# Optimization experiments

Measured on AMD Instinct MI355X. Metric: run time of the kernel, lower is better.

## Reference

```python
import jax, jax.numpy as jnp
import numpy as np

N = 1_000_000      # total points
G = 256            # number of interaction clusters (segments)
D_IN = 4           # [energy, x, y, z] per-point features
H1, H2, LATENT = 64, 128, 256
D_OUT = 3          # vertex position dims


def setup_inputs() -> dict:
    key = jax.random.key(0)
    ks = jax.random.split(key, 10)
    point_cloud = jax.random.normal(ks[0], (N, 5), dtype=jnp.float32)
    seg_ids = jnp.sort(jax.random.randint(ks[1], (N,), 0, G, dtype=jnp.int64))
    def lin(k, fan_in, fan_out):
        s = 1.0 / np.sqrt(fan_in)
        return jax.random.uniform(k, (fan_in, fan_out), jnp.float32, -s, s)
    W1 = lin(ks[2], D_IN, H1);   b1 = jnp.zeros((H1,), jnp.float32)
    W2 = lin(ks[3], H1, H2);     b2 = jnp.zeros((H2,), jnp.float32)
    W3 = lin(ks[4], H2, LATENT); b3 = jnp.zeros((LATENT,), jnp.float32)
    Wf = lin(ks[5], LATENT, D_OUT); bf = jnp.zeros((D_OUT,), jnp.float32)
    return {"point_cloud": point_cloud, "W1": W1, "b1": b1, "W2": W2, "b2": b2,
            "W3": W3, "b3": b3, "Wf": Wf, "bf": bf, "seg_ids": seg_ids}


def reference(point_cloud, W1, b1, W2, b2, W3, b3, Wf, bf, seg_ids):
    pos = point_cloud[:, 1:4]          # [N,3]
    x = point_cloud[:, 4:5]            # [N,1] energy
    # --- per-segment centroids (segment mean, single pass) ---
    counts = jax.ops.segment_sum(jnp.ones((pos.shape[0],), pos.dtype), seg_ids,
                                 num_segments=G)                      # [G]
    centroids = jax.ops.segment_sum(pos, seg_ids, num_segments=G)
    centroids = centroids / jnp.maximum(counts, 1.0)[:, None]         # [G,3]
    # --- PointNet encoder: shared per-point MLP + per-segment max-pool ---
    feats = jnp.concatenate([x, pos], axis=1)                         # [N,4]
    h = jax.nn.relu(feats @ W1 + b1)                                  # [N,64]
    h = jax.nn.relu(h @ W2 + b2)                                      # [N,128]
    h = h @ W3 + b3                                                   # [N,256]
    pooled = jax.ops.segment_max(h, seg_ids, num_segments=G)          # [G,256]
    # --- final Linear + Softplus head, added to centroids ---
    out = jax.nn.softplus(pooled @ Wf + bf)                           # [G,3]
    return centroids + out
```

## Files before the change

kernel.cpp:

```cpp
#include <hip/hip_runtime.h>
#include <float.h>

typedef __bf16 bf16x8 __attribute__((ext_vector_type(8)));
typedef __bf16 bf16x4 __attribute__((ext_vector_type(4)));
typedef float  f32x4  __attribute__((ext_vector_type(4)));

#define G      256
#define MT     32
#define H1DIM  64
#define H2DIM  128
#define LAT    256
#define H1PAD  72
#define H2PAD  136

__device__ __forceinline__ unsigned mapf(float f) {
  unsigned u = __float_as_uint(f);
  return (u & 0x80000000u) ? ~u : (u | 0x80000000u);
}
__device__ __forceinline__ float unmapf(unsigned u) {
  return (u & 0x80000000u) ? __uint_as_float(u & 0x7fffffffu) : __uint_as_float(~u);
}

__device__ __forceinline__ void flush4(f32x4 v0, f32x4 v1, f32x4 v2, f32x4 v3,
                                       int s, int w, int q, int nn,
                                       const float* __restrict__ b3,
                                       unsigned* __restrict__ pooled) {
  f32x4 vv[4] = {v0, v1, v2, v3};
  #pragma unroll
  for (int mt = 0; mt < 4; ++mt)
    #pragma unroll
    for (int r = 0; r < 4; ++r) {
      int feat = w * 64 + mt * 16 + q * 4 + r;
      float v = vv[mt][r] + b3[feat];
      v = fmaxf(v, __shfl_xor(v, 1));
      v = fmaxf(v, __shfl_xor(v, 2));
      v = fmaxf(v, __shfl_xor(v, 4));
      v = fmaxf(v, __shfl_xor(v, 8));
      if (nn == 0) atomicMax(&pooled[s * LAT + feat], mapf(v));
    }
}

__global__ __launch_bounds__(256, 2) void mlp_kernel(
    const float* __restrict__ pc,
    const float* __restrict__ W1, const float* __restrict__ b1,
    const float* __restrict__ W2, const float* __restrict__ b2,
    const float* __restrict__ W3, const float* __restrict__ b3,
    const int* __restrict__ sid,
    unsigned* __restrict__ pooled,
    float* __restrict__ sums,
    int n, int tiles_per_block) {
  __shared__ __align__(16) __bf16 shF[MT][8];
  __shared__ __align__(16) __bf16 sh1[MT][H1PAD];
  __shared__ __align__(16) __bf16 sh2[MT][H2PAD];
  __shared__ int segt[MT];

  const int t  = threadIdx.x;
  const int w  = t >> 6;
  const int lane = t & 63;
  const int q  = lane >> 4;
  const int nn = lane & 15;

  bf16x8 w1f;
  #pragma unroll
  for (int j = 0; j < 8; ++j) {
    int k = q * 8 + j;
    w1f[j] = (k < 4) ? (__bf16)W1[k * H1DIM + w * 16 + nn] : (__bf16)0.f;
  }
  float b1r[4];
  #pragma unroll
  for (int r = 0; r < 4; ++r) b1r[r] = b1[w * 16 + q * 4 + r];

  bf16x8 w2f[2][2];
  float  b2r[2][4];
  #pragma unroll
  for (int mt = 0; mt < 2; ++mt) {
    int m = w * 32 + mt * 16 + nn;
    #pragma unroll
    for (int ks = 0; ks < 2; ++ks)
      #pragma unroll
      for (int j = 0; j < 8; ++j)
        w2f[mt][ks][j] = (__bf16)W2[(ks * 32 + q * 8 + j) * H2DIM + m];
    #pragma unroll
    for (int r = 0; r < 4; ++r) b2r[mt][r] = b2[w * 32 + mt * 16 + q * 4 + r];
  }

  bf16x8 w3f[4][4];
  #pragma unroll
  for (int mt = 0; mt < 4; ++mt) {
    int m = w * 64 + mt * 16 + nn;
    #pragma unroll
    for (int ks = 0; ks < 4; ++ks)
      #pragma unroll
      for (int j = 0; j < 8; ++j)
        w3f[mt][ks][j] = (__bf16)W3[(ks * 32 + q * 8 + j) * LAT + m];
  }

  const f32x4 zero4 = {0.f, 0.f, 0.f, 0.f};
  const bf16x8 zero8 = {};
  const f32x4 neginf4 = {-FLT_MAX, -FLT_MAX, -FLT_MAX, -FLT_MAX};

  f32x4 run[4];
  #pragma unroll
  for (int mt = 0; mt < 4; ++mt) run[mt] = neginf4;

  float cx = 0.f, cy = 0.f, cz = 0.f, cc = 0.f;
  int   cseg = -1;

  const int tile0 = blockIdx.x * tiles_per_block;
  int first = tile0 * MT; if (first > n - 1) first = n - 1;
  int s_cur = sid[first];

  for (int ti = 0; ti < tiles_per_block; ++ti) {
    const int base = (tile0 + ti) * MT;
    if (base >= n) break;

    if (t < MT) {
      int p = base + t;
      bool valid = p < n;
      int pcl = valid ? p : (n - 1);
      const float* pp = pc + (size_t)pcl * 5;
      float fx = pp[4], p1 = pp[1], p2 = pp[2], p3 = pp[3];
      bf16x8 v = {};
      v[0] = (__bf16)fx;
      v[1] = (__bf16)p1;
      v[2] = (__bf16)p2;
      v[3] = (__bf16)p3;
      *reinterpret_cast<bf16x8*>(&shF[t][0]) = v;
      int s = sid[pcl];
      segt[t] = s;
      if (valid) {
        if (s != cseg) {
          if (cc > 0.f) {
            atomicAdd(&sums[cseg * 4 + 0], cx);
            atomicAdd(&sums[cseg * 4 + 1], cy);
            atomicAdd(&sums[cseg * 4 + 2], cz);
            atomicAdd(&sums[cseg * 4 + 3], cc);
          }
          cseg = s; cx = 0.f; cy = 0.f; cz = 0.f; cc = 0.f;
        }
        cx += p1; cy += p2; cz += p3; cc += 1.f;
      }
    }
    __syncthreads();

    {
      f32x4 acc1[2];
      #pragma unroll
      for (int nt = 0; nt < 2; ++nt) {
        bf16x8 ld = *reinterpret_cast<const bf16x8*>(&shF[nt * 16 + nn][0]);
        bf16x8 af = (q == 0) ? ld : zero8;
        acc1[nt] = __builtin_amdgcn_mfma_f32_16x16x32_bf16(w1f, af, zero4, 0, 0, 0);
      }
      #pragma unroll
      for (int nt = 0; nt < 2; ++nt) {
        bf16x4 pk;
        #pragma unroll
        for (int r = 0; r < 4; ++r)
          pk[r] = (__bf16)fmaxf(acc1[nt][r] + b1r[r], 0.f);
        *reinterpret_cast<bf16x4*>(&sh1[nt * 16 + nn][w * 16 + q * 4]) = pk;
      }
    }
    __syncthreads();

    {
      f32x4 acc2[2][2];
      #pragma unroll
      for (int mt = 0; mt < 2; ++mt)
        #pragma unroll
        for (int nt = 0; nt < 2; ++nt) acc2[mt][nt] = zero4;
      #pragma unroll
      for (int ks = 0; ks < 2; ++ks) {
        bf16x8 bfr[2];
        #pragma unroll
        for (int nt = 0; nt < 2; ++nt)
          bfr[nt] = *reinterpret_cast<const bf16x8*>(&sh1[nt * 16 + nn][ks * 32 + q * 8]);
        #pragma unroll
        for (int mt = 0; mt < 2; ++mt)
          #pragma unroll
          for (int nt = 0; nt < 2; ++nt)
            acc2[mt][nt] = __builtin_amdgcn_mfma_f32_16x16x32_bf16(w2f[mt][ks], bfr[nt], acc2[mt][nt], 0, 0, 0);
      }
      #pragma unroll
      for (int mt = 0; mt < 2; ++mt)
        #pragma unroll
        for (int nt = 0; nt < 2; ++nt) {
          bf16x4 pk;
          #pragma unroll
          for (int r = 0; r < 4; ++r)
            pk[r] = (__bf16)fmaxf(acc2[mt][nt][r] + b2r[mt][r], 0.f);
          *reinterpret_cast<bf16x4*>(&sh2[nt * 16 + nn][w * 32 + mt * 16 + q * 4]) = pk;
        }
    }
    __syncthreads();

    f32x4 acc3[4][2];
    #pragma unroll
    for (int mt = 0; mt < 4; ++mt)
      #pragma unroll
      for (int nt = 0; nt < 2; ++nt) acc3[mt][nt] = zero4;
    #pragma unroll
    for (int ks = 0; ks < 4; ++ks) {
      bf16x8 bfr[2];
      #pragma unroll
      for (int nt = 0; nt < 2; ++nt)
        bfr[nt] = *reinterpret_cast<const bf16x8*>(&sh2[nt * 16 + nn][ks * 32 + q * 8]);
      #pragma unroll
      for (int mt = 0; mt < 4; ++mt)
        #pragma unroll
        for (int nt = 0; nt < 2; ++nt)
          acc3[mt][nt] = __builtin_amdgcn_mfma_f32_16x16x32_bf16(w3f[mt][ks], bfr[nt], acc3[mt][nt], 0, 0, 0);
    }

    int smin = segt[0], smax = segt[MT - 1];
    if (smin != s_cur) {
      flush4(run[0], run[1], run[2], run[3], s_cur, w, q, nn, b3, pooled);
      #pragma unroll
      for (int mt = 0; mt < 4; ++mt) run[mt] = neginf4;
      s_cur = smin;
    }
    if (smin == smax) {
      #pragma unroll
      for (int mt = 0; mt < 4; ++mt)
        #pragma unroll
        for (int r = 0; r < 4; ++r)
          run[mt][r] = fmaxf(run[mt][r], fmaxf(acc3[mt][0][r], acc3[mt][1][r]));
    } else {
      int sg0 = segt[nn], sg1 = segt[16 + nn];
      for (int s = smin; s <= smax; ++s) {
        f32x4 tmp[4];
        #pragma unroll
        for (int mt = 0; mt < 4; ++mt)
          #pragma unroll
          for (int r = 0; r < 4; ++r) {
            float v0 = (sg0 == s) ? acc3[mt][0][r] : -FLT_MAX;
            float v1 = (sg1 == s) ? acc3[mt][1][r] : -FLT_MAX;
            tmp[mt][r] = fmaxf(v0, v1);
          }
        if (s < smax) {
          if (s == s_cur) {
            #pragma unroll
            for (int mt = 0; mt < 4; ++mt)
              #pragma unroll
              for (int r = 0; r < 4; ++r) run[mt][r] = fmaxf(run[mt][r], tmp[mt][r]);
            flush4(run[0], run[1], run[2], run[3], s, w, q, nn, b3, pooled);
            #pragma unroll
            for (int mt = 0; mt < 4; ++mt) run[mt] = neginf4;
          } else {
            flush4(tmp[0], tmp[1], tmp[2], tmp[3], s, w, q, nn, b3, pooled);
          }
        } else {
          #pragma unroll
          for (int mt = 0; mt < 4; ++mt)
            #pragma unroll
            for (int r = 0; r < 4; ++r) run[mt][r] = fmaxf(run[mt][r], tmp[mt][r]);
        }
      }
      s_cur = smax;
    }
    __syncthreads();
  }
  flush4(run[0], run[1], run[2], run[3], s_cur, w, q, nn, b3, pooled);

  if (t < MT && cc > 0.f) {
    atomicAdd(&sums[cseg * 4 + 0], cx);
    atomicAdd(&sums[cseg * 4 + 1], cy);
    atomicAdd(&sums[cseg * 4 + 2], cz);
    atomicAdd(&sums[cseg * 4 + 3], cc);
  }
}

__global__ void final_kernel(const float* __restrict__ sums, const unsigned* __restrict__ pooled,
                             const float* __restrict__ Wf, const float* __restrict__ bfv,
                             float* __restrict__ out) {
  __shared__ float red[4][3];
  int g = blockIdx.x;
  int t = threadIdx.x;
  unsigned u = pooled[g * LAT + t];
  float f = u ? unmapf(u) : 0.f;
  float s0 = f * Wf[t * 3 + 0];
  float s1 = f * Wf[t * 3 + 1];
  float s2 = f * Wf[t * 3 + 2];
  #pragma unroll
  for (int off = 1; off < 64; off <<= 1) {
    s0 += __shfl_xor(s0, off);
    s1 += __shfl_xor(s1, off);
    s2 += __shfl_xor(s2, off);
  }
  int wave = t >> 6;
  if ((t & 63) == 0) { red[wave][0] = s0; red[wave][1] = s1; red[wave][2] = s2; }
  __syncthreads();
  if (t < 3) {
    float acc = bfv[t] + red[0][t] + red[1][t] + red[2][t] + red[3][t];
    float sp  = fmaxf(acc, 0.f) + log1pf(expf(-fabsf(acc)));
    float cnt = fmaxf(sums[g * 4 + 3], 1.f);
    float cen = sums[g * 4 + t] / cnt;
    out[g * 3 + t] = cen + sp;
  }
}

extern "C" void kernel_launch(void* const* d_in, const int* in_sizes, int n_in,
                              void* d_out, int out_size, void* d_ws, size_t ws_size,
                              hipStream_t stream) {
  const float* pc  = (const float*)d_in[0];
  const float* W1  = (const float*)d_in[1];
  const float* b1  = (const float*)d_in[2];
  const float* W2  = (const float*)d_in[3];
  const float* b2  = (const float*)d_in[4];
  const float* W3  = (const float*)d_in[5];
  const float* b3  = (const float*)d_in[6];
  const float* Wf  = (const float*)d_in[7];
  const float* bfv = (const float*)d_in[8];
  const int*   sid = (const int*)d_in[9];
  int n = in_sizes[0] / 5;

  float*    sums   = (float*)d_ws;
  unsigned* pooled = (unsigned*)((char*)d_ws + 4096);
  hipMemsetAsync(d_ws, 0, 4096 + (size_t)G * LAT * 4, stream);

  int tiles   = (n + MT - 1) / MT;
  int nblocks = 512;
  int tpb     = (tiles + nblocks - 1) / nblocks;
  mlp_kernel<<<nblocks, 256, 0, stream>>>(pc, W1, b1, W2, b2, W3, b3, sid, pooled, sums, n, tpb);

  final_kernel<<<G, 256, 0, stream>>>(sums, pooled, Wf, bfv, (float*)d_out);
}
```

Measured before the change: 224.9 us.

## Double the point tile to 64 and prefetch next tile's inputs into double-buffered shared memory

Raises the per-iteration tile from 32 to 64 points, so each wave issues more MFMAs per barrier and each weight fragment is reused across more columns. It also double-buffers the input features and segment-id arrays, loading the next tile's point data into registers before the MLP and writing it to the alternate buffer afterwards, removing one barrier per tile and hiding global load latency. The cost is more accumulator registers (acc3 grows to 16 vectors), which may pressure occupancy under launch_bounds(256,2). The host's tiles_per_block or grid size may need to account for the new tile size.

```diff
diff --git a/kernel.cpp b/kernel.cpp
--- a/kernel.cpp
+++ b/kernel.cpp
@@ -6,7 +6,7 @@
 typedef float  f32x4  __attribute__((ext_vector_type(4)));
 
 #define G      256
-#define MT     32
+#define MT     64
 #define H1DIM  64
 #define H2DIM  128
 #define LAT    256
@@ -49,10 +49,10 @@
     unsigned* __restrict__ pooled,
     float* __restrict__ sums,
     int n, int tiles_per_block) {
-  __shared__ __align__(16) __bf16 shF[MT][8];
+  __shared__ __align__(16) __bf16 shF[2][MT][8];
   __shared__ __align__(16) __bf16 sh1[MT][H1PAD];
   __shared__ __align__(16) __bf16 sh2[MT][H2PAD];
-  __shared__ int segt[MT];
+  __shared__ int segt[2][MT];
 
   const int t  = threadIdx.x;
   const int w  = t >> 6;
@@ -110,49 +110,50 @@
   int first = tile0 * MT; if (first > n - 1) first = n - 1;
   int s_cur = sid[first];
 
+  if (t < MT) {
+    int p = tile0 * MT + t;
+    bool valid = p < n;
+    int pcl = valid ? p : (n - 1);
+    const float* pp = pc + (size_t)pcl * 5;
+    float fx = pp[4], p1 = pp[1], p2 = pp[2], p3 = pp[3];
+    bf16x8 v = {};
+    v[0] = (__bf16)fx; v[1] = (__bf16)p1; v[2] = (__bf16)p2; v[3] = (__bf16)p3;
+    *reinterpret_cast<bf16x8*>(&shF[0][t][0]) = v;
+    int s = sid[pcl];
+    segt[0][t] = s;
+    if (valid) { cseg = s; cx = p1; cy = p2; cz = p3; cc = 1.f; }
+  }
+  __syncthreads();
+
+  int cur = 0;
   for (int ti = 0; ti < tiles_per_block; ++ti) {
     const int base = (tile0 + ti) * MT;
     if (base >= n) break;
 
-    if (t < MT) {
-      int p = base + t;
-      bool valid = p < n;
-      int pcl = valid ? p : (n - 1);
+    float pf1 = 0.f, pf2 = 0.f, pf3 = 0.f, pfx = 0.f;
+    int   pfs = 0;
+    bool  pfvalid = false;
+    const int base2 = base + MT;
+    const bool hasNext = (ti + 1 < tiles_per_block) && (base2 < n);
+    if (hasNext && t < MT) {
+      int p = base2 + t;
+      pfvalid = p < n;
+      int pcl = pfvalid ? p : (n - 1);
       const float* pp = pc + (size_t)pcl * 5;
-      float fx = pp[4], p1 = pp[1], p2 = pp[2], p3 = pp[3];
-      bf16x8 v = {};
-      v[0] = (__bf16)fx;
-      v[1] = (__bf16)p1;
-      v[2] = (__bf16)p2;
-      v[3] = (__bf16)p3;
-      *reinterpret_cast<bf16x8*>(&shF[t][0]) = v;
-      int s = sid[pcl];
-      segt[t] = s;
-      if (valid) {
-        if (s != cseg) {
-          if (cc > 0.f) {
-            atomicAdd(&sums[cseg * 4 + 0], cx);
-            atomicAdd(&sums[cseg * 4 + 1], cy);
-            atomicAdd(&sums[cseg * 4 + 2], cz);
-            atomicAdd(&sums[cseg * 4 + 3], cc);
-          }
-          cseg = s; cx = 0.f; cy = 0.f; cz = 0.f; cc = 0.f;
-        }
-        cx += p1; cy += p2; cz += p3; cc += 1.f;
-      }
-    }
-    __syncthreads();
+      pfx = pp[4]; pf1 = pp[1]; pf2 = pp[2]; pf3 = pp[3];
+      pfs = sid[pcl];
+    }
 
     {
-      f32x4 acc1[2];
-      #pragma unroll
-      for (int nt = 0; nt < 2; ++nt) {
-        bf16x8 ld = *reinterpret_cast<const bf16x8*>(&shF[nt * 16 + nn][0]);
+      f32x4 acc1[4];
+      #pragma unroll
+      for (int nt = 0; nt < 4; ++nt) {
+        bf16x8 ld = *reinterpret_cast<const bf16x8*>(&shF[cur][nt * 16 + nn][0]);
         bf16x8 af = (q == 0) ? ld : zero8;
         acc1[nt] = __builtin_amdgcn_mfma_f32_16x16x32_bf16(w1f, af, zero4, 0, 0, 0);
       }
       #pragma unroll
-      for (int nt = 0; nt < 2; ++nt) {
+      for (int nt = 0; nt < 4; ++nt) {
         bf16x4 pk;
         #pragma unroll
         for (int r = 0; r < 4; ++r)
@@ -163,27 +164,27 @@
     __syncthreads();
 
     {
-      f32x4 acc2[2][2];
+      f32x4 acc2[2][4];
       #pragma unroll
       for (int mt = 0; mt < 2; ++mt)
         #pragma unroll
-        for (int nt = 0; nt < 2; ++nt) acc2[mt][nt] = zero4;
+        for (int nt = 0; nt < 4; ++nt) acc2[mt][nt] = zero4;
       #pragma unroll
       for (int ks = 0; ks < 2; ++ks) {
-        bf16x8 bfr[2];
-        #pragma unroll
-        for (int nt = 0; nt < 2; ++nt)
+        bf16x8 bfr[4];
+        #pragma unroll
+        for (int nt = 0; nt < 4; ++nt)
           bfr[nt] = *reinterpret_cast<const bf16x8*>(&sh1[nt * 16 + nn][ks * 32 + q * 8]);
         #pragma unroll
         for (int mt = 0; mt < 2; ++mt)
           #pragma unroll
-          for (int nt = 0; nt < 2; ++nt)
+          for (int nt = 0; nt < 4; ++nt)
             acc2[mt][nt] = __builtin_amdgcn_mfma_f32_16x16x32_bf16(w2f[mt][ks], bfr[nt], acc2[mt][nt], 0, 0, 0);
       }
       #pragma unroll
       for (int mt = 0; mt < 2; ++mt)
         #pragma unroll
-        for (int nt = 0; nt < 2; ++nt) {
+        for (int nt = 0; nt < 4; ++nt) {
           bf16x4 pk;
           #pragma unroll
           for (int r = 0; r < 4; ++r)
@@ -193,25 +194,25 @@
     }
     __syncthreads();
 
-    f32x4 acc3[4][2];
+    f32x4 acc3[4][4];
     #pragma unroll
     for (int mt = 0; mt < 4; ++mt)
       #pragma unroll
-      for (int nt = 0; nt < 2; ++nt) acc3[mt][nt] = zero4;
+      for (int nt = 0; nt < 4; ++nt) acc3[mt][nt] = zero4;
     #pragma unroll
     for (int ks = 0; ks < 4; ++ks) {
-      bf16x8 bfr[2];
-      #pragma unroll
-      for (int nt = 0; nt < 2; ++nt)
+      bf16x8 bfr[4];
+      #pragma unroll
+      for (int nt = 0; nt < 4; ++nt)
         bfr[nt] = *reinterpret_cast<const bf16x8*>(&sh2[nt * 16 + nn][ks * 32 + q * 8]);
       #pragma unroll
       for (int mt = 0; mt < 4; ++mt)
         #pragma unroll
-        for (int nt = 0; nt < 2; ++nt)
+        for (int nt = 0; nt < 4; ++nt)
           acc3[mt][nt] = __builtin_amdgcn_mfma_f32_16x16x32_bf16(w3f[mt][ks], bfr[nt], acc3[mt][nt], 0, 0, 0);
     }
 
-    int smin = segt[0], smax = segt[MT - 1];
+    int smin = segt[cur][0], smax = segt[cur][MT - 1];
     if (smin != s_cur) {
       flush4(run[0], run[1], run[2], run[3], s_cur, w, q, nn, b3, pooled);
       #pragma unroll
@@ -222,10 +223,14 @@
       #pragma unroll
       for (int mt = 0; mt < 4; ++mt)
         #pragma unroll
-        for (int r = 0; r < 4; ++r)
-          run[mt][r] = fmaxf(run[mt][r], fmaxf(acc3[mt][0][r], acc3[mt][1][r]));
+        for (int r = 0; r < 4; ++r) {
+          float m01 = fmaxf(acc3[mt][0][r], acc3[mt][1][r]);
+          float m23 = fmaxf(acc3[mt][2][r], acc3[mt][3][r]);
+          run[mt][r] = fmaxf(run[mt][r], fmaxf(m01, m23));
+        }
     } else {
-      int sg0 = segt[nn], sg1 = segt[16 + nn];
+      int sg0 = segt[cur][nn], sg1 = segt[cur][16 + nn];
+      int sg2 = segt[cur][32 + nn], sg3 = segt[cur][48 + nn];
       for (int s = smin; s <= smax; ++s) {
         f32x4 tmp[4];
         #pragma unroll
@@ -234,7 +239,9 @@
           for (int r = 0; r < 4; ++r) {
             float v0 = (sg0 == s) ? acc3[mt][0][r] : -FLT_MAX;
             float v1 = (sg1 == s) ? acc3[mt][1][r] : -FLT_MAX;
-            tmp[mt][r] = fmaxf(v0, v1);
+            float v2 = (sg2 == s) ? acc3[mt][2][r] : -FLT_MAX;
+            float v3 = (sg3 == s) ? acc3[mt][3][r] : -FLT_MAX;
+            tmp[mt][r] = fmaxf(fmaxf(v0, v1), fmaxf(v2, v3));
           }
         if (s < smax) {
           if (s == s_cur) {
@@ -257,7 +264,27 @@
       }
       s_cur = smax;
     }
+
+    if (hasNext && t < MT) {
+      bf16x8 v = {};
+      v[0] = (__bf16)pfx; v[1] = (__bf16)pf1; v[2] = (__bf16)pf2; v[3] = (__bf16)pf3;
+      *reinterpret_cast<bf16x8*>(&shF[cur ^ 1][t][0]) = v;
+      segt[cur ^ 1][t] = pfs;
+      if (pfvalid) {
+        if (pfs != cseg) {
+          if (cc > 0.f) {
+            atomicAdd(&sums[cseg * 4 + 0], cx);
+            atomicAdd(&sums[cseg * 4 + 1], cy);
+            atomicAdd(&sums[cseg * 4 + 2], cz);
+            atomicAdd(&sums[cseg * 4 + 3], cc);
+          }
+          cseg = pfs; cx = 0.f; cy = 0.f; cz = 0.f; cc = 0.f;
+        }
+        cx += pf1; cy += pf2; cz += pf3; cc += 1.f;
+      }
+    }
     __syncthreads();
+    cur ^= 1;
   }
   flush4(run[0], run[1], run[2], run[3], s_cur, w, q, nn, b3, pooled);
 
```

Result: slower. 289.4 us (+28.7%).

## Cut register pressure to fit three blocks per CU and launch more blocks

Applied to the files above, without the earlier changes.

Raises launch bounds to three blocks per SM/CU and grows the grid from 512 to 768 blocks. To free registers, it folds b1 into the layer-1 MFMA through a constant-1 input column, moves b2 into shared memory, and keeps the per-thread centroid accumulators in shared memory instead of registers. The aim is more resident waves to hide latency. In exchange it adds LDS traffic for the centroid sums and loses some b1 precision, since the bias now passes through bf16.

```diff
diff --git a/kernel.cpp b/kernel.cpp
--- a/kernel.cpp
+++ b/kernel.cpp
@@ -40,7 +40,7 @@
     }
 }
 
-__global__ __launch_bounds__(256, 2) void mlp_kernel(
+__global__ __launch_bounds__(256, 3) void mlp_kernel(
     const float* __restrict__ pc,
     const float* __restrict__ W1, const float* __restrict__ b1,
     const float* __restrict__ W2, const float* __restrict__ b2,
@@ -52,7 +52,10 @@
   __shared__ __align__(16) __bf16 shF[MT][8];
   __shared__ __align__(16) __bf16 sh1[MT][H1PAD];
   __shared__ __align__(16) __bf16 sh2[MT][H2PAD];
-  __shared__ int segt[MT];
+  __shared__ int   segt[MT];
+  __shared__ __align__(16) float shB2[H2DIM];
+  __shared__ float shC[MT][5];
+  __shared__ int   shCseg[MT];
 
   const int t  = threadIdx.x;
   const int w  = t >> 6;
@@ -64,14 +67,12 @@
   #pragma unroll
   for (int j = 0; j < 8; ++j) {
     int k = q * 8 + j;
-    w1f[j] = (k < 4) ? (__bf16)W1[k * H1DIM + w * 16 + nn] : (__bf16)0.f;
-  }
-  float b1r[4];
-  #pragma unroll
-  for (int r = 0; r < 4; ++r) b1r[r] = b1[w * 16 + q * 4 + r];
+    float wv = (k < 4) ? W1[k * H1DIM + w * 16 + nn]
+             : (k == 4 ? b1[w * 16 + nn] : 0.f);
+    w1f[j] = (__bf16)wv;
+  }
 
   bf16x8 w2f[2][2];
-  float  b2r[2][4];
   #pragma unroll
   for (int mt = 0; mt < 2; ++mt) {
     int m = w * 32 + mt * 16 + nn;
@@ -80,8 +81,6 @@
       #pragma unroll
       for (int j = 0; j < 8; ++j)
         w2f[mt][ks][j] = (__bf16)W2[(ks * 32 + q * 8 + j) * H2DIM + m];
-    #pragma unroll
-    for (int r = 0; r < 4; ++r) b2r[mt][r] = b2[w * 32 + mt * 16 + q * 4 + r];
   }
 
   bf16x8 w3f[4][4];
@@ -94,6 +93,9 @@
       for (int j = 0; j < 8; ++j)
         w3f[mt][ks][j] = (__bf16)W3[(ks * 32 + q * 8 + j) * LAT + m];
   }
+
+  if (t < H2DIM) shB2[t] = b2[t];
+  if (t < MT) { shCseg[t] = -1; shC[t][0] = 0.f; shC[t][1] = 0.f; shC[t][2] = 0.f; shC[t][3] = 0.f; }
 
   const f32x4 zero4 = {0.f, 0.f, 0.f, 0.f};
   const bf16x8 zero8 = {};
@@ -102,9 +104,6 @@
   f32x4 run[4];
   #pragma unroll
   for (int mt = 0; mt < 4; ++mt) run[mt] = neginf4;
-
-  float cx = 0.f, cy = 0.f, cz = 0.f, cc = 0.f;
-  int   cseg = -1;
 
   const int tile0 = blockIdx.x * tiles_per_block;
   int first = tile0 * MT; if (first > n - 1) first = n - 1;
@@ -125,20 +124,25 @@
       v[1] = (__bf16)p1;
       v[2] = (__bf16)p2;
       v[3] = (__bf16)p3;
+      v[4] = (__bf16)1.0f;
       *reinterpret_cast<bf16x8*>(&shF[t][0]) = v;
       int s = sid[pcl];
       segt[t] = s;
       if (valid) {
-        if (s != cseg) {
-          if (cc > 0.f) {
-            atomicAdd(&sums[cseg * 4 + 0], cx);
-            atomicAdd(&sums[cseg * 4 + 1], cy);
-            atomicAdd(&sums[cseg * 4 + 2], cz);
-            atomicAdd(&sums[cseg * 4 + 3], cc);
+        int pseg = shCseg[t];
+        if (s != pseg) {
+          float pcnt = shC[t][3];
+          if (pcnt > 0.f) {
+            atomicAdd(&sums[pseg * 4 + 0], shC[t][0]);
+            atomicAdd(&sums[pseg * 4 + 1], shC[t][1]);
+            atomicAdd(&sums[pseg * 4 + 2], shC[t][2]);
+            atomicAdd(&sums[pseg * 4 + 3], pcnt);
           }
-          cseg = s; cx = 0.f; cy = 0.f; cz = 0.f; cc = 0.f;
+          shCseg[t] = s;
+          shC[t][0] = p1; shC[t][1] = p2; shC[t][2] = p3; shC[t][3] = 1.f;
+        } else {
+          shC[t][0] += p1; shC[t][1] += p2; shC[t][2] += p3; shC[t][3] += 1.f;
         }
-        cx += p1; cy += p2; cz += p3; cc += 1.f;
       }
     }
     __syncthreads();
@@ -156,7 +160,7 @@
         bf16x4 pk;
         #pragma unroll
         for (int r = 0; r < 4; ++r)
-          pk[r] = (__bf16)fmaxf(acc1[nt][r] + b1r[r], 0.f);
+          pk[r] = (__bf16)fmaxf(acc1[nt][r], 0.f);
         *reinterpret_cast<bf16x4*>(&sh1[nt * 16 + nn][w * 16 + q * 4]) = pk;
       }
     }
@@ -181,15 +185,17 @@
             acc2[mt][nt] = __builtin_amdgcn_mfma_f32_16x16x32_bf16(w2f[mt][ks], bfr[nt], acc2[mt][nt], 0, 0, 0);
       }
       #pragma unroll
-      for (int mt = 0; mt < 2; ++mt)
+      for (int mt = 0; mt < 2; ++mt) {
+        f32x4 b2v = *reinterpret_cast<const f32x4*>(&shB2[w * 32 + mt * 16 + q * 4]);
         #pragma unroll
         for (int nt = 0; nt < 2; ++nt) {
           bf16x4 pk;
           #pragma unroll
           for (int r = 0; r < 4; ++r)
-            pk[r] = (__bf16)fmaxf(acc2[mt][nt][r] + b2r[mt][r], 0.f);
+            pk[r] = (__bf16)fmaxf(acc2[mt][nt][r] + b2v[r], 0.f);
           *reinterpret_cast<bf16x4*>(&sh2[nt * 16 + nn][w * 32 + mt * 16 + q * 4]) = pk;
         }
+      }
     }
     __syncthreads();
 
@@ -261,11 +267,15 @@
   }
   flush4(run[0], run[1], run[2], run[3], s_cur, w, q, nn, b3, pooled);
 
-  if (t < MT && cc > 0.f) {
-    atomicAdd(&sums[cseg * 4 + 0], cx);
-    atomicAdd(&sums[cseg * 4 + 1], cy);
-    atomicAdd(&sums[cseg * 4 + 2], cz);
-    atomicAdd(&sums[cseg * 4 + 3], cc);
+  if (t < MT) {
+    int pseg = shCseg[t];
+    float pcnt = shC[t][3];
+    if (pseg >= 0 && pcnt > 0.f) {
+      atomicAdd(&sums[pseg * 4 + 0], shC[t][0]);
+      atomicAdd(&sums[pseg * 4 + 1], shC[t][1]);
+      atomicAdd(&sums[pseg * 4 + 2], shC[t][2]);
+      atomicAdd(&sums[pseg * 4 + 3], pcnt);
+    }
   }
 }
 
@@ -318,7 +328,7 @@
   hipMemsetAsync(d_ws, 0, 4096 + (size_t)G * LAT * 4, stream);
 
   int tiles   = (n + MT - 1) / MT;
-  int nblocks = 512;
+  int nblocks = 768;
   int tpb     = (tiles + nblocks - 1) / nblocks;
   mlp_kernel<<<nblocks, 256, 0, stream>>>(pc, W1, b1, W2, b2, W3, b3, sid, pooled, sums, n, tpb);
 
```

Result: slower. 300.4 us (+33.5%).
